# Kernel tuning notes

Measured on AMD Instinct MI355X. Metric: run time of the kernel, lower is better.

The kernel has to match this reference:

```python
import jax, jax.numpy as jnp
import numpy as np

N_NODES = 50000
N_EDGES = 800000
N_GRAPHS = 64
F_IN, H1, H2, H3, N_CLS = 128, 512, 256, 128, 10
BN_EPS = 1e-5


def setup_inputs() -> dict:
    key = jax.random.key(0)
    ks = jax.random.split(key, 16)

    def lin(k, fi, fo):
        return jax.random.normal(k, (fi, fo), jnp.float32) / np.sqrt(fi).astype(np.float32)

    return {
        "x": jax.random.normal(ks[0], (N_NODES, F_IN), jnp.float32),
        "edge_index": jax.random.randint(ks[1], (2, N_EDGES), 0, N_NODES),
        "batch": jnp.sort(jax.random.randint(ks[2], (N_NODES,), 0, N_GRAPHS)),
        "W1": lin(ks[3], F_IN, H1), "b1": jnp.zeros((H1,), jnp.float32),
        "g1": jnp.ones((H1,), jnp.float32), "be1": jnp.zeros((H1,), jnp.float32),
        "W2": lin(ks[4], H1, H2), "b2": jnp.zeros((H2,), jnp.float32),
        "g2": jnp.ones((H2,), jnp.float32), "be2": jnp.zeros((H2,), jnp.float32),
        "W3": lin(ks[5], H2, H3), "b3": jnp.zeros((H3,), jnp.float32),
        "g3": jnp.ones((H3,), jnp.float32), "be3": jnp.zeros((H3,), jnp.float32),
        "Wo": lin(ks[6], H3, N_CLS), "bo": jnp.zeros((N_CLS,), jnp.float32),
    }


def _gcn_conv(x, row, col, W, b):
    # PyG GCNConv: h = x @ W; add self-loops; sym-normalized scatter-add; + bias
    n = x.shape[0]
    h = x @ W
    loop = jnp.arange(n, dtype=row.dtype)
    row2 = jnp.concatenate([row, loop])  # source nodes
    col2 = jnp.concatenate([col, loop])  # target nodes
    deg = jax.ops.segment_sum(jnp.ones_like(col2, dtype=h.dtype), col2, num_segments=n)
    dinv = jnp.where(deg > 0, jax.lax.rsqrt(deg), 0.0)
    norm = (dinv[row2] * dinv[col2])[:, None]
    agg = jax.ops.segment_sum(h[row2] * norm, col2, num_segments=n)
    return agg + b


def _bn(x, g, b):
    # training-mode BatchNorm over node dim (biased variance, eps=1e-5)
    mean = jnp.mean(x, axis=0)
    var = jnp.mean(jnp.square(x - mean), axis=0)
    return g * (x - mean) * jax.lax.rsqrt(var + BN_EPS) + b


def reference(x, edge_index, batch, W1, b1, g1, be1, W2, b2, g2, be2,
              W3, b3, g3, be3, Wo, bo):
    row, col = edge_index[0], edge_index[1]
    h = jax.nn.relu(_bn(_gcn_conv(x, row, col, W1, b1), g1, be1))
    h = jax.nn.relu(_bn(_gcn_conv(h, row, col, W2, b2), g2, be2))
    h = jax.nn.relu(_bn(_gcn_conv(h, row, col, W3, b3), g3, be3))
    # global_mean_pool over graph ids
    sums = jax.ops.segment_sum(h, batch, num_segments=N_GRAPHS)
    cnt = jax.ops.segment_sum(jnp.ones((h.shape[0],), h.dtype), batch, num_segments=N_GRAPHS)
    pooled = sums / jnp.maximum(cnt, 1.0)[:, None]
    return pooled @ Wo + bo
```

## Files before the change

kernel.cpp:

```cpp
#include <hip/hip_runtime.h>
#include <hip/hip_bf16.h>
#include <cstdint>
#include <cstddef>

#define NNODES 50000
#define NGRAPHS 64

typedef short bf16x8 __attribute__((ext_vector_type(8)));
typedef float f32x4 __attribute__((ext_vector_type(4)));

__device__ inline float bf2f(unsigned short u) {
    return __uint_as_float(((unsigned)u) << 16);
}
__device__ inline unsigned short f2bf(float f) {
    unsigned u = __float_as_uint(f);
    return (unsigned short)((u + 0x7fff + ((u >> 16) & 1)) >> 16);
}

__global__ void deg_count_k(const int* __restrict__ col, int* __restrict__ cnt, int ne) {
    int i = blockIdx.x * blockDim.x + threadIdx.x;
    if (i < ne) atomicAdd(&cnt[col[i]], 1);
}

__global__ __launch_bounds__(256) void scan1_k(const int* __restrict__ cnt, int* __restrict__ offs,
                                               int* __restrict__ bsum, float* __restrict__ dinv, int n) {
    int t = threadIdx.x;
    int base = blockIdx.x * 1024 + t * 4;
    int4 v = {0, 0, 0, 0};
    if (base + 3 < n) v = *reinterpret_cast<const int4*>(cnt + base);
    else {
        if (base + 0 < n) v.x = cnt[base + 0];
        if (base + 1 < n) v.y = cnt[base + 1];
        if (base + 2 < n) v.z = cnt[base + 2];
    }
    if (base + 0 < n) dinv[base + 0] = rsqrtf((float)(v.x + 1));
    if (base + 1 < n) dinv[base + 1] = rsqrtf((float)(v.y + 1));
    if (base + 2 < n) dinv[base + 2] = rsqrtf((float)(v.z + 1));
    if (base + 3 < n) dinv[base + 3] = rsqrtf((float)(v.w + 1));

    int s = v.x + v.y + v.z + v.w;
    __shared__ int lds[256];
    lds[t] = s;
    __syncthreads();
    #pragma unroll
    for (int d = 1; d < 256; d <<= 1) {
        int u = (t >= d) ? lds[t - d] : 0;
        __syncthreads();
        lds[t] += u;
        __syncthreads();
    }
    int excl = lds[t] - s;
    if (t == 255) bsum[blockIdx.x] = lds[t];

    if (base + 3 < n) {
        int4 o;
        o.x = excl; o.y = excl + v.x; o.z = o.y + v.y; o.w = o.z + v.z;
        *reinterpret_cast<int4*>(offs + base) = o;
    } else {
        int e = excl;
        if (base + 0 < n) { offs[base + 0] = e; e += v.x; }
        if (base + 1 < n) { offs[base + 1] = e; e += v.y; }
        if (base + 2 < n) { offs[base + 2] = e; }
    }
}

__global__ __launch_bounds__(256) void scan2_k(int* __restrict__ bsum, int nb) {
    __shared__ int lds[256];
    int t = threadIdx.x;
    int v = (t < nb) ? bsum[t] : 0;
    lds[t] = v;
    __syncthreads();
    #pragma unroll
    for (int d = 1; d < 256; d <<= 1) {
        int u = (t >= d) ? lds[t - d] : 0;
        __syncthreads();
        lds[t] += u;
        __syncthreads();
    }
    if (t < nb) bsum[t] = lds[t] - v;
}

__global__ __launch_bounds__(256) void scan3_k(int* __restrict__ offs, const int* __restrict__ bsum, int n) {
    int base = blockIdx.x * 1024 + threadIdx.x * 4;
    int add = bsum[blockIdx.x];
    if (base + 3 < n) {
        int4 o = *reinterpret_cast<int4*>(offs + base);
        o.x += add; o.y += add; o.z += add; o.w += add;
        *reinterpret_cast<int4*>(offs + base) = o;
    } else {
        for (int k = 0; k < 4; ++k)
            if (base + k < n) offs[base + k] += add;
    }
}

__global__ void scatter_k(const int* __restrict__ row_, const int* __restrict__ col_,
                          const int* __restrict__ offs, int* __restrict__ fill,
                          int* __restrict__ csr_row, int ne) {
    int e = blockIdx.x * blockDim.x + threadIdx.x;
    if (e >= ne) return;
    int r = row_[e], c = col_[e];
    int pos = offs[c] + atomicAdd(&fill[c], 1);
    csr_row[pos] = r;
}

__global__ void cvt_scale_k(const float* __restrict__ in, const float* __restrict__ dinv,
                            unsigned short* __restrict__ out, int n) {
    long long i = (long long)blockIdx.x * blockDim.x + threadIdx.x;
    long long total4 = (long long)n * 32;
    if (i >= total4) return;
    int r = (int)(i >> 5);
    float d = dinv[r];
    float4 v = reinterpret_cast<const float4*>(in)[i];
    uint2 o;
    o.x = (unsigned)f2bf(v.x * d) | ((unsigned)f2bf(v.y * d) << 16);
    o.y = (unsigned)f2bf(v.z * d) | ((unsigned)f2bf(v.w * d) << 16);
    reinterpret_cast<uint2*>(out)[i] = o;
}

__global__ void wtrans_k(const float* __restrict__ W, unsigned short* __restrict__ Wt, int K, int M) {
    int idx = blockIdx.x * blockDim.x + threadIdx.x;
    if (idx >= K * M) return;
    int k = idx / M, m = idx - k * M;
    Wt[(size_t)m * K + k] = f2bf(W[idx]);
}

template<int FC>
__device__ inline void loadrow(const unsigned short* __restrict__ p, float* v) {
    if constexpr (FC == 2) {
        unsigned u = *reinterpret_cast<const unsigned*>(p);
        v[0] = bf2f((unsigned short)(u & 0xffff));
        v[1] = bf2f((unsigned short)(u >> 16));
    } else {
        uint2 u = *reinterpret_cast<const uint2*>(p);
        v[0] = bf2f((unsigned short)(u.x & 0xffff));
        v[1] = bf2f((unsigned short)(u.x >> 16));
        v[2] = bf2f((unsigned short)(u.y & 0xffff));
        v[3] = bf2f((unsigned short)(u.y >> 16));
    }
}

template<int FC>
__global__ void agg_s_k(const unsigned short* __restrict__ in, const int* __restrict__ offs,
                        const int* __restrict__ cnt, const int* __restrict__ csr_row,
                        const float* __restrict__ dinv, unsigned short* __restrict__ out, int n) {
    const int F = 64 * FC;
    int node = blockIdx.x * (blockDim.x >> 6) + (threadIdx.x >> 6);
    if (node >= n) return;
    int lane = threadIdx.x & 63;
    const size_t foff = (size_t)lane * FC;

    float acc[FC];
    loadrow<FC>(in + (size_t)node * F + foff, acc);

    int s = offs[node], e1 = s + cnt[node];
    int e = s;
    for (; e + 4 <= e1; e += 4) {
        int r0 = csr_row[e], r1 = csr_row[e + 1], r2 = csr_row[e + 2], r3 = csr_row[e + 3];
        float v0[FC], v1[FC], v2[FC], v3[FC];
        loadrow<FC>(in + (size_t)r0 * F + foff, v0);
        loadrow<FC>(in + (size_t)r1 * F + foff, v1);
        loadrow<FC>(in + (size_t)r2 * F + foff, v2);
        loadrow<FC>(in + (size_t)r3 * F + foff, v3);
        #pragma unroll
        for (int i = 0; i < FC; ++i) acc[i] += (v0[i] + v1[i]) + (v2[i] + v3[i]);
    }
    for (; e < e1; ++e) {
        int r0 = csr_row[e];
        float v0[FC];
        loadrow<FC>(in + (size_t)r0 * F + foff, v0);
        #pragma unroll
        for (int i = 0; i < FC; ++i) acc[i] += v0[i];
    }

    float d = dinv[node];
    unsigned short* q = out + (size_t)node * F + foff;
    if constexpr (FC == 2) {
        unsigned o = (unsigned)f2bf(acc[0] * d) | ((unsigned)f2bf(acc[1] * d) << 16);
        *reinterpret_cast<unsigned*>(q) = o;
    } else {
        uint2 o;
        o.x = (unsigned)f2bf(acc[0] * d) | ((unsigned)f2bf(acc[1] * d) << 16);
        o.y = (unsigned)f2bf(acc[2] * d) | ((unsigned)f2bf(acc[3] * d) << 16);
        *reinterpret_cast<uint2*>(q) = o;
    }
}

template<bool BN_A, bool SCALE_OUT, bool STATS>
__global__ __launch_bounds__(256) void gemm_bt_k(const unsigned short* __restrict__ A,
                                                 const unsigned short* __restrict__ B,
                                                 unsigned short* __restrict__ C,
                                                 const float* __restrict__ scale,
                                                 const float* __restrict__ shift,
                                                 const float* __restrict__ dinv,
                                                 float* __restrict__ sums,
                                                 float* __restrict__ sqs,
                                                 int n, int K, int M) {
    __shared__ unsigned short As[128][40];
    __shared__ unsigned short Bs[128][40];
    int tid = threadIdx.x;
    int wid = tid >> 6, lane = tid & 63;
    int wr = wid >> 1, wc = wid & 1;
    int row0 = blockIdx.y * 128, col0 = blockIdx.x * 128;

    f32x4 acc[4][4] = {};

    for (int kt = 0; kt < K; kt += 32) {
        int c8 = (tid & 3) * 8;
        float4 sc0, sc1, sh0, sh1;
        if (BN_A) {
            sc0 = *reinterpret_cast<const float4*>(scale + kt + c8);
            sc1 = *reinterpret_cast<const float4*>(scale + kt + c8 + 4);
            sh0 = *reinterpret_cast<const float4*>(shift + kt + c8);
            sh1 = *reinterpret_cast<const float4*>(shift + kt + c8 + 4);
        }
        #pragma unroll
        for (int h = 0; h < 2; ++h) {
            int r = (tid >> 2) + h * 64;
            int gr = row0 + r;
            bf16x8 va = {};
            if (gr < n) va = *reinterpret_cast<const bf16x8*>(A + (size_t)gr * K + kt + c8);
            if (BN_A) {
                #pragma unroll
                for (int t = 0; t < 8; ++t) {
                    float sct = (t < 4) ? (&sc0.x)[t] : (&sc1.x)[t - 4];
                    float sht = (t < 4) ? (&sh0.x)[t] : (&sh1.x)[t - 4];
                    float f = bf2f((unsigned short)va[t]);
                    va[t] = (short)f2bf(fmaxf(f * sct + sht, 0.f));
                }
            }
            *reinterpret_cast<bf16x8*>(&As[r][c8]) = va;
            bf16x8 vb = *reinterpret_cast<const bf16x8*>(B + (size_t)(col0 + r) * K + kt + c8);
            *reinterpret_cast<bf16x8*>(&Bs[r][c8]) = vb;
        }
        __syncthreads();

        bf16x8 af[4], bfr[4];
        int koff = (lane >> 4) * 8;
        #pragma unroll
        for (int f = 0; f < 4; ++f) {
            af[f]  = *reinterpret_cast<const bf16x8*>(&As[wr * 64 + f * 16 + (lane & 15)][koff]);
            bfr[f] = *reinterpret_cast<const bf16x8*>(&Bs[wc * 64 + f * 16 + (lane & 15)][koff]);
        }
        #pragma unroll
        for (int i = 0; i < 4; ++i)
            #pragma unroll
            for (int j = 0; j < 4; ++j)
                acc[i][j] = __builtin_amdgcn_mfma_f32_16x16x32_bf16(af[i], bfr[j], acc[i][j], 0, 0, 0);
        __syncthreads();
    }

    #pragma unroll
    for (int i = 0; i < 4; ++i) {
        #pragma unroll
        for (int q = 0; q < 4; ++q) {
            int gr = row0 + wr * 64 + i * 16 + (lane >> 4) * 4 + q;
            if (gr < n) {
                float dr = SCALE_OUT ? dinv[gr] : 1.0f;
                #pragma unroll
                for (int j = 0; j < 4; ++j) {
                    int gc = col0 + wc * 64 + j * 16 + (lane & 15);
                    C[(size_t)gr * M + gc] = f2bf(acc[i][j][q] * dr);
                }
            }
        }
    }

    if (STATS) {
        #pragma unroll
        for (int j = 0; j < 4; ++j) {
            float s = 0.f, q = 0.f;
            #pragma unroll
            for (int i = 0; i < 4; ++i)
                #pragma unroll
                for (int p = 0; p < 4; ++p) {
                    float v = acc[i][j][p];
                    s += v; q += v * v;
                }
            s += __shfl_xor(s, 16, 64); s += __shfl_xor(s, 32, 64);
            q += __shfl_xor(q, 16, 64); q += __shfl_xor(q, 32, 64);
            if ((lane >> 4) == 0) {
                int gc = col0 + wc * 64 + j * 16 + (lane & 15);
                atomicAdd(&sums[gc], s);
                atomicAdd(&sqs[gc], q);
            }
        }
    }
}

template<int F>
__global__ __launch_bounds__(256) void bn_stats_k(const unsigned short* __restrict__ in,
                                                  float* __restrict__ stat, int n) {
    constexpr int G   = F / 8;
    constexpr int RPP = 256 / G;
    int g  = threadIdx.x & (G - 1);
    int rl = threadIdx.x / G;

    float s[8] = {}, q[8] = {};
    for (int r = blockIdx.x * RPP + rl; r < n; r += gridDim.x * RPP) {
        uint4 u = *reinterpret_cast<const uint4*>(in + (size_t)r * F + g * 8);
        float v[8];
        v[0] = bf2f((unsigned short)(u.x & 0xffff)); v[1] = bf2f((unsigned short)(u.x >> 16));
        v[2] = bf2f((unsigned short)(u.y & 0xffff)); v[3] = bf2f((unsigned short)(u.y >> 16));
        v[4] = bf2f((unsigned short)(u.z & 0xffff)); v[5] = bf2f((unsigned short)(u.z >> 16));
        v[6] = bf2f((unsigned short)(u.w & 0xffff)); v[7] = bf2f((unsigned short)(u.w >> 16));
        #pragma unroll
        for (int i = 0; i < 8; ++i) { s[i] += v[i]; q[i] += v[i] * v[i]; }
    }

    __shared__ float lds[RPP][F];
    #pragma unroll
    for (int i = 0; i < 8; ++i) lds[rl][g * 8 + i] = s[i];
    __syncthreads();
    if (threadIdx.x < F) {
        float t = 0.f;
        #pragma unroll
        for (int rr = 0; rr < RPP; ++rr) t += lds[rr][threadIdx.x];
        atomicAdd(&stat[threadIdx.x], t);
    }
    __syncthreads();
    #pragma unroll
    for (int i = 0; i < 8; ++i) lds[rl][g * 8 + i] = q[i];
    __syncthreads();
    if (threadIdx.x < F) {
        float t = 0.f;
        #pragma unroll
        for (int rr = 0; rr < RPP; ++rr) t += lds[rr][threadIdx.x];
        atomicAdd(&stat[F + threadIdx.x], t);
    }
}

__global__ void bn_finalize_k(const float* __restrict__ stat,
                              const float* __restrict__ g, const float* __restrict__ be,
                              float* __restrict__ scale, float* __restrict__ shift,
                              int F, float invn) {
    int f = blockIdx.x * blockDim.x + threadIdx.x;
    if (f >= F) return;
    float mean = stat[f] * invn;
    float var  = stat[F + f] * invn - mean * mean;
    float rstd = rsqrtf(var + 1e-5f);
    float sc = g[f] * rstd;
    scale[f] = sc;
    shift[f] = be[f] - mean * sc;
}

__global__ void bounds_k(const int* __restrict__ batch, int* __restrict__ start, int n) {
    int i = blockIdx.x * blockDim.x + threadIdx.x;
    if (i >= n) return;
    int b = batch[i];
    if (i == 0) {
        for (int g = 0; g <= b; ++g) start[g] = 0;
    } else {
        int pb = batch[i - 1];
        for (int g = pb + 1; g <= b; ++g) start[g] = i;
    }
    if (i == n - 1) {
        for (int g = b + 1; g <= NGRAPHS; ++g) start[g] = n;
    }
}

__global__ __launch_bounds__(256) void pool_part_k(const unsigned short* __restrict__ a,
                                                   const int* __restrict__ start,
                                                   const float* __restrict__ scale,
                                                   const float* __restrict__ shift,
                                                   float* __restrict__ partial) {
    int g = blockIdx.x, q = blockIdx.y;
    int s = start[g], e = start[g + 1];
    int nr = e - s;
    int c0 = s + (nr * q) / 4, c1 = s + (nr * (q + 1)) / 4;
    int tf = threadIdx.x & 15, tr = threadIdx.x >> 4;

    float sc[8], sh[8];
    #pragma unroll
    for (int i = 0; i < 8; ++i) { sc[i] = scale[tf * 8 + i]; sh[i] = shift[tf * 8 + i]; }

    float acc[8] = {};
    for (int r = c0 + tr; r < c1; r += 16) {
        uint4 u = *reinterpret_cast<const uint4*>(a + (size_t)r * 128 + tf * 8);
        float v[8];
        v[0] = bf2f((unsigned short)(u.x & 0xffff)); v[1] = bf2f((unsigned short)(u.x >> 16));
        v[2] = bf2f((unsigned short)(u.y & 0xffff)); v[3] = bf2f((unsigned short)(u.y >> 16));
        v[4] = bf2f((unsigned short)(u.z & 0xffff)); v[5] = bf2f((unsigned short)(u.z >> 16));
        v[6] = bf2f((unsigned short)(u.w & 0xffff)); v[7] = bf2f((unsigned short)(u.w >> 16));
        #pragma unroll
        for (int i = 0; i < 8; ++i) acc[i] += fmaxf(v[i] * sc[i] + sh[i], 0.f);
    }

    __shared__ float red[16][128];
    #pragma unroll
    for (int i = 0; i < 8; ++i) red[tr][tf * 8 + i] = acc[i];
    __syncthreads();
    int f = threadIdx.x;
    if (f < 128) {
        float s2 = 0.f;
        #pragma unroll
        for (int t = 0; t < 16; ++t) s2 += red[t][f];
        partial[((size_t)(g * 4 + q)) * 128 + f] = s2;
    }
}

__global__ void final_out_k(const float* __restrict__ partial, const int* __restrict__ start,
                            const float* __restrict__ Wo, const float* __restrict__ bo,
                            float* __restrict__ out) {
    int idx = blockIdx.x * blockDim.x + threadIdx.x;
    if (idx >= NGRAPHS * 10) return;
    int g = idx / 10, c = idx - g * 10;
    float cntf = (float)(start[g + 1] - start[g]);
    float inv = 1.0f / fmaxf(cntf, 1.0f);
    float s = bo[c];
    for (int k = 0; k < 128; ++k) {
        float pk = partial[(size_t)(g * 4 + 0) * 128 + k] + partial[(size_t)(g * 4 + 1) * 128 + k]
                 + partial[(size_t)(g * 4 + 2) * 128 + k] + partial[(size_t)(g * 4 + 3) * 128 + k];
        s += pk * inv * Wo[k * 10 + c];
    }
    out[idx] = s;
}

extern "C" void kernel_launch(void* const* d_in, const int* in_sizes, int n_in,
                              void* d_out, int out_size, void* d_ws, size_t ws_size,
                              hipStream_t stream) {
    const float* x   = (const float*)d_in[0];
    const int*   ei  = (const int*)d_in[1];
    const int*   bat = (const int*)d_in[2];
    const float* W1  = (const float*)d_in[3];
    const float* g1  = (const float*)d_in[5];
    const float* be1 = (const float*)d_in[6];
    const float* W2  = (const float*)d_in[7];
    const float* g2  = (const float*)d_in[9];
    const float* be2 = (const float*)d_in[10];
    const float* W3  = (const float*)d_in[11];
    const float* g3  = (const float*)d_in[13];
    const float* be3 = (const float*)d_in[14];
    const float* Wo  = (const float*)d_in[15];
    const float* bo  = (const float*)d_in[16];
    float* out = (float*)d_out;

    const int n  = in_sizes[2];
    const int ne = in_sizes[1] / 2;
    const int* row = ei;
    const int* col = ei + ne;
    const int NB = (n + 1023) / 1024;

    char* base = (char*)d_ws;
    size_t o = 0;
    auto alloc = [&](size_t bytes) -> char* {
        char* p = base + o;
        o += (bytes + 255) & ~(size_t)255;
        return p;
    };
    int*   cntfill = (int*)alloc((size_t)2 * n * 4);
    int*   cnt  = cntfill;
    int*   fill = cntfill + n;
    int*   offs  = (int*)alloc(n * 4);
    int*   bsum  = (int*)alloc(256 * 4);
    float* dinv  = (float*)alloc(n * 4);
    int*   start = (int*)alloc((NGRAPHS + 1) * 4);
    float* stat  = (float*)alloc(1024 * 4);
    float* scale = (float*)alloc(512 * 4);
    float* shift = (float*)alloc(512 * 4);
    float* partial = (float*)alloc((size_t)NGRAPHS * 4 * 128 * 4);
    int*   csr_row = (int*)alloc((size_t)ne * 4);
    unsigned short* Wt1 = (unsigned short*)alloc((size_t)128 * 512 * 2);
    unsigned short* Wt2 = (unsigned short*)alloc((size_t)512 * 256 * 2);
    unsigned short* Wt3 = (unsigned short*)alloc((size_t)256 * 128 * 2);
    unsigned short* xs_bf  = (unsigned short*)alloc((size_t)n * 128 * 2);
    unsigned short* ax_bf  = (unsigned short*)alloc((size_t)n * 128 * 2);
    unsigned short* h1_bf  = (unsigned short*)alloc((size_t)n * 512 * 2);
    unsigned short* t2s_bf = (unsigned short*)alloc((size_t)n * 256 * 2);
    unsigned short* a2_bf  = (unsigned short*)alloc((size_t)n * 256 * 2);
    unsigned short* t3s_bf = (unsigned short*)alloc((size_t)n * 128 * 2);
    unsigned short* a3_bf  = (unsigned short*)alloc((size_t)n * 128 * 2);

    hipMemsetAsync(cntfill, 0, (size_t)2 * n * sizeof(int), stream);
    deg_count_k<<<(ne + 255) / 256, 256, 0, stream>>>(col, cnt, ne);
    scan1_k<<<NB, 256, 0, stream>>>(cnt, offs, bsum, dinv, n);
    scan2_k<<<1, 256, 0, stream>>>(bsum, NB);
    scan3_k<<<NB, 256, 0, stream>>>(offs, bsum, n);
    scatter_k<<<(ne + 255) / 256, 256, 0, stream>>>(row, col, offs, fill, csr_row, ne);
    bounds_k<<<(n + 255) / 256, 256, 0, stream>>>(bat, start, n);

    cvt_scale_k<<<(unsigned)(((long long)n * 32 + 255) / 256), 256, 0, stream>>>(x, dinv, xs_bf, n);
    wtrans_k<<<(128 * 512 + 255) / 256, 256, 0, stream>>>(W1, Wt1, 128, 512);
    wtrans_k<<<(512 * 256 + 255) / 256, 256, 0, stream>>>(W2, Wt2, 512, 256);
    wtrans_k<<<(256 * 128 + 255) / 256, 256, 0, stream>>>(W3, Wt3, 256, 128);

    agg_s_k<2><<<(n + 3) / 4, 256, 0, stream>>>(xs_bf, offs, cnt, csr_row, dinv, ax_bf, n);
    hipMemsetAsync(stat, 0, 1024 * sizeof(float), stream);
    gemm_bt_k<false, false, true><<<dim3(4, (n + 127) / 128), 256, 0, stream>>>(
        ax_bf, Wt1, h1_bf, nullptr, nullptr, nullptr, stat, stat + 512, n, 128, 512);
    bn_finalize_k<<<2, 256, 0, stream>>>(stat, g1, be1, scale, shift, 512, 1.0f / n);

    gemm_bt_k<true, true, false><<<dim3(2, (n + 127) / 128), 256, 0, stream>>>(
        h1_bf, Wt2, t2s_bf, scale, shift, dinv, nullptr, nullptr, n, 512, 256);
    agg_s_k<4><<<(n + 3) / 4, 256, 0, stream>>>(t2s_bf, offs, cnt, csr_row, dinv, a2_bf, n);
    hipMemsetAsync(stat, 0, 1024 * sizeof(float), stream);
    bn_stats_k<256><<<1024, 256, 0, stream>>>(a2_bf, stat, n);
    bn_finalize_k<<<1, 256, 0, stream>>>(stat, g2, be2, scale, shift, 256, 1.0f / n);

    gemm_bt_k<true, true, false><<<dim3(1, (n + 127) / 128), 256, 0, stream>>>(
        a2_bf, Wt3, t3s_bf, scale, shift, dinv, nullptr, nullptr, n, 256, 128);
    agg_s_k<2><<<(n + 3) / 4, 256, 0, stream>>>(t3s_bf, offs, cnt, csr_row, dinv, a3_bf, n);
    hipMemsetAsync(stat, 0, 1024 * sizeof(float), stream);
    bn_stats_k<128><<<1024, 256, 0, stream>>>(a3_bf, stat, n);
    bn_finalize_k<<<1, 256, 0, stream>>>(stat, g3, be3, scale, shift, 128, 1.0f / n);

    pool_part_k<<<dim3(NGRAPHS, 4), 256, 0, stream>>>(a3_bf, start, scale, shift, partial);
    final_out_k<<<3, 256, 0, stream>>>(partial, start, Wo, bo, out);
}
```

Before: 527.4 us.

## Widen aggregation gathers to 16-byte loads with lane-group edge parallelism

```diff
diff --git a/kernel.cpp b/kernel.cpp
--- a/kernel.cpp
+++ b/kernel.cpp
@@ -15,6 +15,12 @@
 __device__ inline unsigned short f2bf(float f) {
     unsigned u = __float_as_uint(f);
     return (unsigned short)((u + 0x7fff + ((u >> 16) & 1)) >> 16);
+}
+__device__ inline void unpack8(uint4 u, float* v) {
+    v[0] = bf2f((unsigned short)(u.x & 0xffff)); v[1] = bf2f((unsigned short)(u.x >> 16));
+    v[2] = bf2f((unsigned short)(u.y & 0xffff)); v[3] = bf2f((unsigned short)(u.y >> 16));
+    v[4] = bf2f((unsigned short)(u.z & 0xffff)); v[5] = bf2f((unsigned short)(u.z >> 16));
+    v[6] = bf2f((unsigned short)(u.w & 0xffff)); v[7] = bf2f((unsigned short)(u.w >> 16));
 }
 
 __global__ void deg_count_k(const int* __restrict__ col, int* __restrict__ cnt, int ne) {
@@ -117,25 +123,22 @@
     reinterpret_cast<uint2*>(out)[i] = o;
 }
 
-__global__ void wtrans_k(const float* __restrict__ W, unsigned short* __restrict__ Wt, int K, int M) {
+__global__ void wtrans_all_k(const float* __restrict__ W1, const float* __restrict__ W2,
+                             const float* __restrict__ W3,
+                             unsigned short* __restrict__ Wt1, unsigned short* __restrict__ Wt2,
+                             unsigned short* __restrict__ Wt3) {
     int idx = blockIdx.x * blockDim.x + threadIdx.x;
-    if (idx >= K * M) return;
-    int k = idx / M, m = idx - k * M;
-    Wt[(size_t)m * K + k] = f2bf(W[idx]);
-}
-
-template<int FC>
-__device__ inline void loadrow(const unsigned short* __restrict__ p, float* v) {
-    if constexpr (FC == 2) {
-        unsigned u = *reinterpret_cast<const unsigned*>(p);
-        v[0] = bf2f((unsigned short)(u & 0xffff));
-        v[1] = bf2f((unsigned short)(u >> 16));
-    } else {
-        uint2 u = *reinterpret_cast<const uint2*>(p);
-        v[0] = bf2f((unsigned short)(u.x & 0xffff));
-        v[1] = bf2f((unsigned short)(u.x >> 16));
-        v[2] = bf2f((unsigned short)(u.y & 0xffff));
-        v[3] = bf2f((unsigned short)(u.y >> 16));
+    if (idx < 65536) {
+        int k = idx >> 9, m = idx & 511;
+        Wt1[m * 128 + k] = f2bf(W1[idx]);
+    } else if (idx < 196608) {
+        int j = idx - 65536;
+        int k = j >> 8, m = j & 255;
+        Wt2[m * 512 + k] = f2bf(W2[j]);
+    } else if (idx < 229376) {
+        int j = idx - 196608;
+        int k = j >> 7, m = j & 127;
+        Wt3[m * 256 + k] = f2bf(W3[j]);
     }
 }
 
@@ -143,45 +146,62 @@
 __global__ void agg_s_k(const unsigned short* __restrict__ in, const int* __restrict__ offs,
                         const int* __restrict__ cnt, const int* __restrict__ csr_row,
                         const float* __restrict__ dinv, unsigned short* __restrict__ out, int n) {
-    const int F = 64 * FC;
-    int node = blockIdx.x * (blockDim.x >> 6) + (threadIdx.x >> 6);
+    constexpr int F   = 64 * FC;
+    constexpr int LPE = (FC == 4) ? 32 : 16;
+    constexpr int EPL = 64 / LPE;
+    int node = blockIdx.x * 4 + (threadIdx.x >> 6);
     if (node >= n) return;
     int lane = threadIdx.x & 63;
-    const size_t foff = (size_t)lane * FC;
-
-    float acc[FC];
-    loadrow<FC>(in + (size_t)node * F + foff, acc);
+    int sub = lane / LPE;
+    int fl  = lane % LPE;
+    const size_t foff = (size_t)fl * 8;
+
+    float acc[8] = {};
+    if (sub == 0) {
+        uint4 u = *reinterpret_cast<const uint4*>(in + (size_t)node * F + foff);
+        float v[8]; unpack8(u, v);
+        #pragma unroll
+        for (int i = 0; i < 8; ++i) acc[i] = v[i];
+    }
 
     int s = offs[node], e1 = s + cnt[node];
-    int e = s;
-    for (; e + 4 <= e1; e += 4) {
-        int r0 = csr_row[e], r1 = csr_row[e + 1], r2 = csr_row[e + 2], r3 = csr_row[e + 3];
-        float v0[FC], v1[FC], v2[FC], v3[FC];
-        loadrow<FC>(in + (size_t)r0 * F + foff, v0);
-        loadrow<FC>(in + (size_t)r1 * F + foff, v1);
-        loadrow<FC>(in + (size_t)r2 * F + foff, v2);
-        loadrow<FC>(in + (size_t)r3 * F + foff, v3);
-        #pragma unroll
-        for (int i = 0; i < FC; ++i) acc[i] += (v0[i] + v1[i]) + (v2[i] + v3[i]);
-    }
-    for (; e < e1; ++e) {
-        int r0 = csr_row[e];
-        float v0[FC];
-        loadrow<FC>(in + (size_t)r0 * F + foff, v0);
-        #pragma unroll
-        for (int i = 0; i < FC; ++i) acc[i] += v0[i];
-    }
-
-    float d = dinv[node];
-    unsigned short* q = out + (size_t)node * F + foff;
-    if constexpr (FC == 2) {
-        unsigned o = (unsigned)f2bf(acc[0] * d) | ((unsigned)f2bf(acc[1] * d) << 16);
-        *reinterpret_cast<unsigned*>(q) = o;
-    } else {
-        uint2 o;
-        o.x = (unsigned)f2bf(acc[0] * d) | ((unsigned)f2bf(acc[1] * d) << 16);
-        o.y = (unsigned)f2bf(acc[2] * d) | ((unsigned)f2bf(acc[3] * d) << 16);
-        *reinterpret_cast<uint2*>(q) = o;
+    int eb = s;
+    for (; eb + 2 * EPL <= e1; eb += 2 * EPL) {
+        int r0 = csr_row[eb + sub];
+        int r1 = csr_row[eb + EPL + sub];
+        uint4 u0 = *reinterpret_cast<const uint4*>(in + (size_t)r0 * F + foff);
+        uint4 u1 = *reinterpret_cast<const uint4*>(in + (size_t)r1 * F + foff);
+        float v0[8], v1[8];
+        unpack8(u0, v0); unpack8(u1, v1);
+        #pragma unroll
+        for (int i = 0; i < 8; ++i) acc[i] += v0[i] + v1[i];
+    }
+    for (; eb < e1; eb += EPL) {
+        int e = eb + sub;
+        bool ok = e < e1;
+        int r = csr_row[ok ? e : e1 - 1];
+        uint4 u = *reinterpret_cast<const uint4*>(in + (size_t)r * F + foff);
+        float v[8]; unpack8(u, v);
+        if (ok) {
+            #pragma unroll
+            for (int i = 0; i < 8; ++i) acc[i] += v[i];
+        }
+    }
+
+    #pragma unroll
+    for (int d = LPE; d < 64; d <<= 1) {
+        #pragma unroll
+        for (int i = 0; i < 8; ++i) acc[i] += __shfl_xor(acc[i], d, 64);
+    }
+
+    if (sub == 0) {
+        float dn = dinv[node];
+        uint4 o;
+        o.x = (unsigned)f2bf(acc[0] * dn) | ((unsigned)f2bf(acc[1] * dn) << 16);
+        o.y = (unsigned)f2bf(acc[2] * dn) | ((unsigned)f2bf(acc[3] * dn) << 16);
+        o.z = (unsigned)f2bf(acc[4] * dn) | ((unsigned)f2bf(acc[5] * dn) << 16);
+        o.w = (unsigned)f2bf(acc[6] * dn) | ((unsigned)f2bf(acc[7] * dn) << 16);
+        *reinterpret_cast<uint4*>(out + (size_t)node * F + foff) = o;
     }
 }
 
@@ -298,11 +318,7 @@
     float s[8] = {}, q[8] = {};
     for (int r = blockIdx.x * RPP + rl; r < n; r += gridDim.x * RPP) {
         uint4 u = *reinterpret_cast<const uint4*>(in + (size_t)r * F + g * 8);
-        float v[8];
-        v[0] = bf2f((unsigned short)(u.x & 0xffff)); v[1] = bf2f((unsigned short)(u.x >> 16));
-        v[2] = bf2f((unsigned short)(u.y & 0xffff)); v[3] = bf2f((unsigned short)(u.y >> 16));
-        v[4] = bf2f((unsigned short)(u.z & 0xffff)); v[5] = bf2f((unsigned short)(u.z >> 16));
-        v[6] = bf2f((unsigned short)(u.w & 0xffff)); v[7] = bf2f((unsigned short)(u.w >> 16));
+        float v[8]; unpack8(u, v);
         #pragma unroll
         for (int i = 0; i < 8; ++i) { s[i] += v[i]; q[i] += v[i] * v[i]; }
     }
@@ -376,11 +392,7 @@
     float acc[8] = {};
     for (int r = c0 + tr; r < c1; r += 16) {
         uint4 u = *reinterpret_cast<const uint4*>(a + (size_t)r * 128 + tf * 8);
-        float v[8];
-        v[0] = bf2f((unsigned short)(u.x & 0xffff)); v[1] = bf2f((unsigned short)(u.x >> 16));
-        v[2] = bf2f((unsigned short)(u.y & 0xffff)); v[3] = bf2f((unsigned short)(u.y >> 16));
-        v[4] = bf2f((unsigned short)(u.z & 0xffff)); v[5] = bf2f((unsigned short)(u.z >> 16));
-        v[6] = bf2f((unsigned short)(u.w & 0xffff)); v[7] = bf2f((unsigned short)(u.w >> 16));
+        float v[8]; unpack8(u, v);
         #pragma unroll
         for (int i = 0; i < 8; ++i) acc[i] += fmaxf(v[i] * sc[i] + sh[i], 0.f);
     }
@@ -450,11 +462,16 @@
     int*   cntfill = (int*)alloc((size_t)2 * n * 4);
     int*   cnt  = cntfill;
     int*   fill = cntfill + n;
+    float* statall = (float*)alloc((size_t)3 * 1024 * 4);
+    float* stat1 = statall;
+    float* stat2 = statall + 1024;
+    float* stat3 = statall + 2048;
+    size_t zspan = (size_t)((char*)(statall + 3 * 1024) - (char*)cntfill);
+
     int*   offs  = (int*)alloc(n * 4);
     int*   bsum  = (int*)alloc(256 * 4);
     float* dinv  = (float*)alloc(n * 4);
     int*   start = (int*)alloc((NGRAPHS + 1) * 4);
-    float* stat  = (float*)alloc(1024 * 4);
     float* scale = (float*)alloc(512 * 4);
     float* shift = (float*)alloc(512 * 4);
     float* partial = (float*)alloc((size_t)NGRAPHS * 4 * 128 * 4);
@@ -470,7 +487,7 @@
     unsigned short* t3s_bf = (unsigned short*)alloc((size_t)n * 128 * 2);
     unsigned short* a3_bf  = (unsigned short*)alloc((size_t)n * 128 * 2);
 
-    hipMemsetAsync(cntfill, 0, (size_t)2 * n * sizeof(int), stream);
+    hipMemsetAsync(cntfill, 0, zspan, stream);
     deg_count_k<<<(ne + 255) / 256, 256, 0, stream>>>(col, cnt, ne);
     scan1_k<<<NB, 256, 0, stream>>>(cnt, offs, bsum, dinv, n);
     scan2_k<<<1, 256, 0, stream>>>(bsum, NB);
@@ -479,29 +496,24 @@
     bounds_k<<<(n + 255) / 256, 256, 0, stream>>>(bat, start, n);
 
     cvt_scale_k<<<(unsigned)(((long long)n * 32 + 255) / 256), 256, 0, stream>>>(x, dinv, xs_bf, n);
-    wtrans_k<<<(128 * 512 + 255) / 256, 256, 0, stream>>>(W1, Wt1, 128, 512);
-    wtrans_k<<<(512 * 256 + 255) / 256, 256, 0, stream>>>(W2, Wt2, 512, 256);
-    wtrans_k<<<(256 * 128 + 255) / 256, 256, 0, stream>>>(W3, Wt3, 256, 128);
+    wtrans_all_k<<<896, 256, 0, stream>>>(W1, W2, W3, Wt1, Wt2, Wt3);
 
     agg_s_k<2><<<(n + 3) / 4, 256, 0, stream>>>(xs_bf, offs, cnt, csr_row, dinv, ax_bf, n);
-    hipMemsetAsync(stat, 0, 1024 * sizeof(float), stream);
     gemm_bt_k<false, false, true><<<dim3(4, (n + 127) / 128), 256, 0, stream>>>(
-        ax_bf, Wt1, h1_bf, nullptr, nullptr, nullptr, stat, stat + 512, n, 128, 512);
-    bn_finalize_k<<<2, 256, 0, stream>>>(stat, g1, be1, scale, shift, 512, 1.0f / n);
+        ax_bf, Wt1, h1_bf, nullptr, nullptr, nullptr, stat1, stat1 + 512, n, 128, 512);
+    bn_finalize_k<<<2, 256, 0, stream>>>(stat1, g1, be1, scale, shift, 512, 1.0f / n);
 
     gemm_bt_k<true, true, false><<<dim3(2, (n + 127) / 128), 256, 0, stream>>>(
         h1_bf, Wt2, t2s_bf, scale, shift, dinv, nullptr, nullptr, n, 512, 256);
     agg_s_k<4><<<(n + 3) / 4, 256, 0, stream>>>(t2s_bf, offs, cnt, csr_row, dinv, a2_bf, n);
-    hipMemsetAsync(stat, 0, 1024 * sizeof(float), stream);
-    bn_stats_k<256><<<1024, 256, 0, stream>>>(a2_bf, stat, n);
-    bn_finalize_k<<<1, 256, 0, stream>>>(stat, g2, be2, scale, shift, 256, 1.0f / n);
+    bn_stats_k<256><<<1024, 256, 0, stream>>>(a2_bf, stat2, n);
+    bn_finalize_k<<<1, 256, 0, stream>>>(stat2, g2, be2, scale, shift, 256, 1.0f / n);
 
     gemm_bt_k<true, true, false><<<dim3(1, (n + 127) / 128), 256, 0, stream>>>(
         a2_bf, Wt3, t3s_bf, scale, shift, dinv, nullptr, nullptr, n, 256, 128);
     agg_s_k<2><<<(n + 3) / 4, 256, 0, stream>>>(t3s_bf, offs, cnt, csr_row, dinv, a3_bf, n);
-    hipMemsetAsync(stat, 0, 1024 * sizeof(float), stream);
-    bn_stats_k<128><<<1024, 256, 0, stream>>>(a3_bf, stat, n);
-    bn_finalize_k<<<1, 256, 0, stream>>>(stat, g3, be3, scale, shift, 128, 1.0f / n);
+    bn_stats_k<128><<<1024, 256, 0, stream>>>(a3_bf, stat3, n);
+    bn_finalize_k<<<1, 256, 0, stream>>>(stat3, g3, be3, scale, shift, 128, 1.0f / n);
 
     pool_part_k<<<dim3(NGRAPHS, 4), 256, 0, stream>>>(a3_bf, start, scale, shift, partial);
     final_out_k<<<3, 256, 0, stream>>>(partial, start, Wo, bo, out);
```

Result: faster. 506.2 us (-4.0%).
